# Kernel optimization log

Measured on AMD Instinct MI355X. Metric: run time of the kernel, lower is better.

Reference implementation:

```python
import jax, jax.numpy as jnp
import numpy as np

B, L, D, I = 64, 196, 2048, 512

def setup_inputs() -> dict:
    key = jax.random.key(0)
    ks = jax.random.split(key, 8)
    s_f = 1.0 / np.sqrt(D)
    s_h = 1.0 / np.sqrt(I)
    s_a = 1.0 / np.sqrt(I)
    return {
        "feature_vectors": jax.random.normal(ks[0], (B, L, D), dtype=jnp.float32),
        "hidden_state": jax.random.normal(ks[1], (B, I), dtype=jnp.float32),
        "W_f": jax.random.uniform(ks[2], (D, I), jnp.float32, -s_f, s_f),
        "b_f": jax.random.uniform(ks[3], (I,), jnp.float32, -s_f, s_f),
        "W_h": jax.random.uniform(ks[4], (I, I), jnp.float32, -s_h, s_h),
        "b_h": jax.random.uniform(ks[5], (I,), jnp.float32, -s_h, s_h),
        "W_a": jax.random.uniform(ks[6], (I, D), jnp.float32, -s_a, s_a),
        "b_a": jax.random.uniform(ks[7], (D,), jnp.float32, -s_a, s_a),
    }

def reference(feature_vectors, hidden_state, W_f, b_f, W_h, b_h, W_a, b_a):
    # fv: [B,L,D], hidden: [B,I]
    fv_shaped = jnp.einsum('bld,di->bli', feature_vectors, W_f) + b_f      # [B,L,I]
    hs_shaped = hidden_state @ W_h + b_h                                   # [B,I]
    e = jnp.einsum('bli,id->bld', fv_shaped + hs_shaped[:, None, :], W_a) + b_a  # [B,L,D]
    alpha = jax.nn.softmax(e, axis=1)                                      # softmax over L locations
    z = jnp.sum(alpha * feature_vectors, axis=1)                           # [B,D] (vectorized loop)
    return (z, alpha)
```

## Files before the change

kernel.cpp:

```cpp
#include <hip/hip_runtime.h>

#define B_ 64
#define L_ 196
#define D_ 2048
#define I_ 512
#define M_ (B_*L_)

typedef __attribute__((ext_vector_type(8))) short bf16x8;
typedef __attribute__((ext_vector_type(4))) float f32x4;
typedef unsigned short u16;

__device__ __forceinline__ u16 f2bf(float x){
  unsigned u = __float_as_uint(x);
  u += 0x7fffu + ((u >> 16) & 1u);
  return (u16)(u >> 16);
}

__device__ __forceinline__ void gld16(const void* g, void* l){
  __builtin_amdgcn_global_load_lds(
      (const __attribute__((address_space(1))) void*)g,
      (__attribute__((address_space(3))) void*)l, 16, 0, 0);
}

__global__ void cvt_bf16_kernel(const float* __restrict__ in, u16* __restrict__ out, int n4){
  int i = blockIdx.x*blockDim.x + threadIdx.x;
  int stride = gridDim.x*blockDim.x;
  for (; i < n4; i += stride){
    float4 v = ((const float4*)in)[i];
    ushort4 o;
    o.x = f2bf(v.x); o.y = f2bf(v.y); o.z = f2bf(v.z); o.w = f2bf(v.w);
    ((ushort4*)out)[i] = o;
  }
}

__global__ void transpose_cvt_kernel(const float* __restrict__ in, u16* __restrict__ out, int R, int C){
  __shared__ float tile[32][33];
  int c0 = blockIdx.x*32, r0 = blockIdx.y*32;
  int tx = threadIdx.x, ty = threadIdx.y;
  for (int i=0;i<32;i+=8)
    tile[ty+i][tx] = in[(size_t)(r0+ty+i)*C + c0 + tx];
  __syncthreads();
  for (int i=0;i<32;i+=8)
    out[(size_t)(c0+ty+i)*R + r0 + tx] = f2bf(tile[tx][ty+i]);
}

__global__ void hs_kernel(const float* __restrict__ hidden, const float* __restrict__ Wh,
                          const float* __restrict__ bh, float* __restrict__ hs){
  int n = blockIdx.x*blockDim.x + threadIdx.x;
  int b = blockIdx.y;
  const float* hrow = hidden + b*I_;
  float a0=0.f,a1=0.f,a2=0.f,a3=0.f;
  for (int k=0;k<I_;k+=4){
    a0 = fmaf(hrow[k+0], Wh[(size_t)(k+0)*I_ + n], a0);
    a1 = fmaf(hrow[k+1], Wh[(size_t)(k+1)*I_ + n], a1);
    a2 = fmaf(hrow[k+2], Wh[(size_t)(k+2)*I_ + n], a2);
    a3 = fmaf(hrow[k+3], Wh[(size_t)(k+3)*I_ + n], a3);
  }
  hs[b*I_ + n] = bh[n] + ((a0+a1)+(a2+a3));
}

template<int BN, int K, int MODE, int NLD>
__launch_bounds__(256)
__global__ void gemm_kernel(const u16* __restrict__ A, const u16* __restrict__ Bt,
                            const float* __restrict__ bias, const float* __restrict__ hs,
                            u16* __restrict__ outb, float* __restrict__ outf)
{
  constexpr int BM = 128, BK = 64;
  constexpr int NF = BN/32;
  constexpr int AW = 4;
  constexpr int BW = BN/32;

  __shared__ __align__(16) u16 Als[BM*BK];
  __shared__ __align__(16) u16 Bls[BN*BK];

  const int tid = threadIdx.x, lane = tid & 63, wave = tid >> 6;
  const int m0 = blockIdx.y * BM, n0 = blockIdx.x * BN;
  const int q = lane >> 4, mr = lane & 15;
  const int wrow = (wave & 1) * 64;
  const int wcol = (wave >> 1) * (BN/2);

  const int lrow = lane >> 3;
  const int kc   = (lane & 7) ^ lrow;

  const u16* Ag[AW]; u16* Al[AW];
  #pragma unroll
  for (int u=0; u<AW; ++u){
    int j = wave*AW + u;
    Ag[u] = A + (size_t)(m0 + j*8 + lrow)*K + kc*8;
    Al[u] = Als + j*512;
  }
  const u16* Bg[BW]; u16* Bl[BW];
  #pragma unroll
  for (int u=0; u<BW; ++u){
    int j = wave*BW + u;
    Bg[u] = Bt + (size_t)(n0 + j*8 + lrow)*K + kc*8;
    Bl[u] = Bls + j*512;
  }

  int aoff[4][2], boff[NF][2];
  #pragma unroll
  for (int i=0;i<4;i++)
    #pragma unroll
    for (int s=0;s<2;s++){
      int R = wrow + i*16 + mr;
      aoff[i][s] = R*64 + (((s*4+q) ^ (mr&7))*8);
    }
  #pragma unroll
  for (int j=0;j<NF;j++)
    #pragma unroll
    for (int s=0;s<2;s++){
      int C = wcol + j*16 + mr;
      boff[j][s] = C*64 + (((s*4+q) ^ (mr&7))*8);
    }

  f32x4 acc[4][NF];
  #pragma unroll
  for (int i=0;i<4;i++)
    #pragma unroll
    for (int j=0;j<NF;j++) acc[i][j] = (f32x4){0.f,0.f,0.f,0.f};

  for (int k0=0; k0<K; k0+=BK){
    __syncthreads();
    #pragma unroll
    for (int u=0;u<AW;++u) gld16(Ag[u] + k0, Al[u]);
    #pragma unroll
    for (int u=0;u<BW;++u) gld16(Bg[u] + k0, Bl[u]);
    __syncthreads();
    #pragma unroll
    for (int s=0;s<2;s++){
      bf16x8 af[4], bg[NF];
      #pragma unroll
      for (int i=0;i<4;i++) af[i] = *(const bf16x8*)(Als + aoff[i][s]);
      #pragma unroll
      for (int j=0;j<NF;j++) bg[j] = *(const bf16x8*)(Bls + boff[j][s]);
      #pragma unroll
      for (int i=0;i<4;i++)
        #pragma unroll
        for (int j=0;j<NF;j++)
          acc[i][j] = __builtin_amdgcn_mfma_f32_16x16x32_bf16(af[i], bg[j], acc[i][j], 0,0,0);
    }
  }

  #pragma unroll
  for (int i=0;i<4;i++){
    #pragma unroll
    for (int j=0;j<NF;j++){
      int gcol = n0 + wcol + j*16 + mr;
      float bcol = bias[gcol];
      #pragma unroll
      for (int r=0;r<4;r++){
        int grow = m0 + wrow + i*16 + q*4 + r;
        float v = acc[i][j][r] + bcol;
        if (MODE == 0){
          int batch = grow / L_;
          outb[(size_t)grow*NLD + gcol] = f2bf(v + hs[batch*I_ + gcol]);
        } else {
          outf[(size_t)grow*NLD + gcol] = v;
        }
      }
    }
  }
}

__launch_bounds__(256)
__global__ void softmax_z_kernel(const float* __restrict__ fv, float* __restrict__ out){
  __shared__ float red[4][64];
  const int dl = threadIdx.x & 63, g = threadIdx.x >> 6;
  const int d = blockIdx.x*64 + dl, b = blockIdx.y;
  float* e = out + (size_t)B_*D_ + (size_t)b*L_*D_ + d;
  const float* f = fv + (size_t)b*L_*D_ + d;

  float ev[49];
  float m = -3.4e38f;
  #pragma unroll
  for (int j=0;j<49;j++){
    ev[j] = e[(size_t)(g*49+j)*D_];
    m = fmaxf(m, ev[j]);
  }
  red[g][dl] = m;
  __syncthreads();
  m = fmaxf(fmaxf(red[0][dl],red[1][dl]), fmaxf(red[2][dl],red[3][dl]));
  __syncthreads();

  float s = 0.f;
  #pragma unroll
  for (int j=0;j<49;j++){ ev[j] = __expf(ev[j]-m); s += ev[j]; }
  red[g][dl] = s;
  __syncthreads();
  s = (red[0][dl]+red[1][dl]) + (red[2][dl]+red[3][dl]);
  __syncthreads();

  float inv = 1.f/s, z = 0.f;
  #pragma unroll
  for (int j=0;j<49;j++){
    float a = ev[j]*inv;
    e[(size_t)(g*49+j)*D_] = a;
    z = fmaf(a, f[(size_t)(g*49+j)*D_], z);
  }
  red[g][dl] = z;
  __syncthreads();
  if (g==0)
    out[(size_t)b*D_ + dl + blockIdx.x*64] = (red[0][dl]+red[1][dl]) + (red[2][dl]+red[3][dl]);
}

extern "C" void kernel_launch(void* const* d_in, const int* in_sizes, int n_in,
                              void* d_out, int out_size, void* d_ws, size_t ws_size,
                              hipStream_t stream){
  (void)in_sizes; (void)n_in; (void)out_size; (void)ws_size;
  const float* fv     = (const float*)d_in[0];
  const float* hidden = (const float*)d_in[1];
  const float* W_f    = (const float*)d_in[2];
  const float* b_f    = (const float*)d_in[3];
  const float* W_h    = (const float*)d_in[4];
  const float* b_h    = (const float*)d_in[5];
  const float* W_a    = (const float*)d_in[6];
  const float* b_a    = (const float*)d_in[7];
  float* out = (float*)d_out;

  char* ws = (char*)d_ws;
  u16*   fv_bf = (u16*)ws;
  u16*   t_bf  = (u16*)(ws + 51380224);
  u16*   WfT   = (u16*)(ws + 64225280);
  u16*   WaT   = (u16*)(ws + 66322432);
  float* hsbuf = (float*)(ws + 68419584);

  cvt_bf16_kernel<<<4096, 256, 0, stream>>>(fv, fv_bf, (B_*L_*D_)/4);
  transpose_cvt_kernel<<<dim3(I_/32, D_/32), dim3(32,8), 0, stream>>>(W_f, WfT, D_, I_);
  transpose_cvt_kernel<<<dim3(D_/32, I_/32), dim3(32,8), 0, stream>>>(W_a, WaT, I_, D_);
  hs_kernel<<<dim3(I_/256, B_), 256, 0, stream>>>(hidden, W_h, b_h, hsbuf);

  gemm_kernel<64, D_, 0, I_><<<dim3(I_/64, M_/128), 256, 0, stream>>>(fv_bf, WfT, b_f, hsbuf, t_bf, nullptr);
  gemm_kernel<128, I_, 1, D_><<<dim3(D_/128, M_/128), 256, 0, stream>>>(t_bf, WaT, b_a, nullptr, nullptr, out + B_*D_);

  softmax_z_kernel<<<dim3(D_/64, B_), 256, 0, stream>>>(fv, out);
}
```

Before: 372.3 us.

## Fuse second GEMM with softmax and weighted sum, double-buffer GEMM loads

```diff
diff --git a/kernel.cpp b/kernel.cpp
--- a/kernel.cpp
+++ b/kernel.cpp
@@ -20,6 +20,18 @@
   __builtin_amdgcn_global_load_lds(
       (const __attribute__((address_space(1))) void*)g,
       (__attribute__((address_space(3))) void*)l, 16, 0, 0);
+}
+
+template<int N> __device__ __forceinline__ void wait_vm(){
+  __builtin_amdgcn_s_waitcnt((N&15) | ((N&48)<<10) | (7<<4) | (15<<8));
+}
+__device__ __forceinline__ void wait_lgkm0(){
+  __builtin_amdgcn_s_waitcnt(15 | (48<<10) | (7<<4));
+}
+__device__ __forceinline__ void bar(){
+  asm volatile("" ::: "memory");
+  __builtin_amdgcn_s_barrier();
+  asm volatile("" ::: "memory");
 }
 
 __global__ void cvt_bf16_kernel(const float* __restrict__ in, u16* __restrict__ out, int n4){
@@ -59,148 +71,238 @@
   hs[b*I_ + n] = bh[n] + ((a0+a1)+(a2+a3));
 }
 
-template<int BN, int K, int MODE, int NLD>
 __launch_bounds__(256)
-__global__ void gemm_kernel(const u16* __restrict__ A, const u16* __restrict__ Bt,
-                            const float* __restrict__ bias, const float* __restrict__ hs,
-                            u16* __restrict__ outb, float* __restrict__ outf)
+__global__ void gemm1_kernel(const u16* __restrict__ A, const u16* __restrict__ Bt,
+                             const float* __restrict__ bias, const float* __restrict__ hs,
+                             u16* __restrict__ outb)
 {
-  constexpr int BM = 128, BK = 64;
-  constexpr int NF = BN/32;
-  constexpr int AW = 4;
-  constexpr int BW = BN/32;
-
-  __shared__ __align__(16) u16 Als[BM*BK];
-  __shared__ __align__(16) u16 Bls[BN*BK];
-
-  const int tid = threadIdx.x, lane = tid & 63, wave = tid >> 6;
-  const int m0 = blockIdx.y * BM, n0 = blockIdx.x * BN;
-  const int q = lane >> 4, mr = lane & 15;
-  const int wrow = (wave & 1) * 64;
-  const int wcol = (wave >> 1) * (BN/2);
-
-  const int lrow = lane >> 3;
-  const int kc   = (lane & 7) ^ lrow;
-
-  const u16* Ag[AW]; u16* Al[AW];
-  #pragma unroll
-  for (int u=0; u<AW; ++u){
-    int j = wave*AW + u;
-    Ag[u] = A + (size_t)(m0 + j*8 + lrow)*K + kc*8;
-    Al[u] = Als + j*512;
-  }
-  const u16* Bg[BW]; u16* Bl[BW];
-  #pragma unroll
-  for (int u=0; u<BW; ++u){
-    int j = wave*BW + u;
-    Bg[u] = Bt + (size_t)(n0 + j*8 + lrow)*K + kc*8;
-    Bl[u] = Bls + j*512;
-  }
-
-  int aoff[4][2], boff[NF][2];
-  #pragma unroll
-  for (int i=0;i<4;i++)
+  constexpr int K = D_, BK = 64, NIT = K/BK;
+  __shared__ __align__(16) u16 Als[2][64*64];
+  __shared__ __align__(16) u16 Bls[2][128*64];
+
+  const int tid = threadIdx.x, lane = tid&63, wave = tid>>6;
+  const int m0 = blockIdx.y*64, n0 = blockIdx.x*128;
+  const int q = lane>>4, mr = lane&15;
+  const int wrow = (wave&1)*32, wcol = (wave>>1)*64;
+  const int lrow = lane>>3, kc = (lane&7)^lrow;
+
+  const u16* Ag[2]; int Alo[2];
+  #pragma unroll
+  for (int u=0;u<2;++u){ int j = wave*2+u; Ag[u] = A + (size_t)(m0 + j*8 + lrow)*K + kc*8; Alo[u] = j*512; }
+  const u16* Bg[4]; int Blo[4];
+  #pragma unroll
+  for (int u=0;u<4;++u){ int j = wave*4+u; Bg[u] = Bt + (size_t)(n0 + j*8 + lrow)*K + kc*8; Blo[u] = j*512; }
+
+  int aoff[2][2], boff[4][2];
+  #pragma unroll
+  for (int i=0;i<2;i++)
+    #pragma unroll
+    for (int s=0;s<2;s++){ int R = wrow + i*16 + mr; aoff[i][s] = R*64 + (((s*4+q) ^ (mr&7))*8); }
+  #pragma unroll
+  for (int j=0;j<4;j++)
+    #pragma unroll
+    for (int s=0;s<2;s++){ int C = wcol + j*16 + mr; boff[j][s] = C*64 + (((s*4+q) ^ (mr&7))*8); }
+
+  f32x4 acc[2][4];
+  #pragma unroll
+  for (int i=0;i<2;i++)
+    #pragma unroll
+    for (int j=0;j<4;j++) acc[i][j] = (f32x4){0.f,0.f,0.f,0.f};
+
+  #pragma unroll
+  for (int u=0;u<2;++u) gld16(Ag[u],    &Als[0][Alo[u]]);
+  #pragma unroll
+  for (int u=0;u<4;++u) gld16(Bg[u],    &Bls[0][Blo[u]]);
+  #pragma unroll
+  for (int u=0;u<2;++u) gld16(Ag[u]+BK, &Als[1][Alo[u]]);
+  #pragma unroll
+  for (int u=0;u<4;++u) gld16(Bg[u]+BK, &Bls[1][Blo[u]]);
+
+  for (int i=0;i<NIT;++i){
+    if (i+1<NIT) wait_vm<6>(); else wait_vm<0>();
+    bar();
+    const u16* Ab = Als[i&1];
+    const u16* Bb = Bls[i&1];
+    bf16x8 af[2][2], bg[4][2];
     #pragma unroll
     for (int s=0;s<2;s++){
-      int R = wrow + i*16 + mr;
-      aoff[i][s] = R*64 + (((s*4+q) ^ (mr&7))*8);
-    }
-  #pragma unroll
-  for (int j=0;j<NF;j++)
-    #pragma unroll
-    for (int s=0;s<2;s++){
-      int C = wcol + j*16 + mr;
-      boff[j][s] = C*64 + (((s*4+q) ^ (mr&7))*8);
-    }
-
-  f32x4 acc[4][NF];
-  #pragma unroll
-  for (int i=0;i<4;i++)
-    #pragma unroll
-    for (int j=0;j<NF;j++) acc[i][j] = (f32x4){0.f,0.f,0.f,0.f};
-
-  for (int k0=0; k0<K; k0+=BK){
-    __syncthreads();
-    #pragma unroll
-    for (int u=0;u<AW;++u) gld16(Ag[u] + k0, Al[u]);
-    #pragma unroll
-    for (int u=0;u<BW;++u) gld16(Bg[u] + k0, Bl[u]);
-    __syncthreads();
-    #pragma unroll
-    for (int s=0;s<2;s++){
-      bf16x8 af[4], bg[NF];
-      #pragma unroll
-      for (int i=0;i<4;i++) af[i] = *(const bf16x8*)(Als + aoff[i][s]);
-      #pragma unroll
-      for (int j=0;j<NF;j++) bg[j] = *(const bf16x8*)(Bls + boff[j][s]);
-      #pragma unroll
-      for (int i=0;i<4;i++)
+      #pragma unroll
+      for (int i2=0;i2<2;i2++) af[i2][s] = *(const bf16x8*)(Ab + aoff[i2][s]);
+      #pragma unroll
+      for (int j=0;j<4;j++)    bg[j][s]  = *(const bf16x8*)(Bb + boff[j][s]);
+    }
+    wait_lgkm0();
+    bar();
+    if (i+2<NIT){
+      int k0 = (i+2)*BK;
+      #pragma unroll
+      for (int u=0;u<2;++u) gld16(Ag[u]+k0, &Als[i&1][Alo[u]]);
+      #pragma unroll
+      for (int u=0;u<4;++u) gld16(Bg[u]+k0, &Bls[i&1][Blo[u]]);
+    }
+    #pragma unroll
+    for (int s=0;s<2;s++)
+      #pragma unroll
+      for (int i2=0;i2<2;i2++)
         #pragma unroll
-        for (int j=0;j<NF;j++)
-          acc[i][j] = __builtin_amdgcn_mfma_f32_16x16x32_bf16(af[i], bg[j], acc[i][j], 0,0,0);
-    }
-  }
-
-  #pragma unroll
-  for (int i=0;i<4;i++){
-    #pragma unroll
-    for (int j=0;j<NF;j++){
+        for (int j=0;j<4;j++)
+          acc[i2][j] = __builtin_amdgcn_mfma_f32_16x16x32_bf16(af[i2][s], bg[j][s], acc[i2][j], 0,0,0);
+  }
+
+  #pragma unroll
+  for (int i2=0;i2<2;i2++){
+    #pragma unroll
+    for (int j=0;j<4;j++){
       int gcol = n0 + wcol + j*16 + mr;
       float bcol = bias[gcol];
       #pragma unroll
       for (int r=0;r<4;r++){
-        int grow = m0 + wrow + i*16 + q*4 + r;
-        float v = acc[i][j][r] + bcol;
-        if (MODE == 0){
-          int batch = grow / L_;
-          outb[(size_t)grow*NLD + gcol] = f2bf(v + hs[batch*I_ + gcol]);
-        } else {
-          outf[(size_t)grow*NLD + gcol] = v;
+        int grow = m0 + wrow + i2*16 + q*4 + r;
+        int batch = grow / L_;
+        outb[(size_t)grow*I_ + gcol] = f2bf(acc[i2][j][r] + bcol + hs[batch*I_ + gcol]);
+      }
+    }
+  }
+}
+
+__launch_bounds__(256)
+__global__ void gemm2_fused_kernel(const u16* __restrict__ T, const u16* __restrict__ Wa,
+                                   const float* __restrict__ b_a, const float* __restrict__ fv,
+                                   float* __restrict__ out)
+{
+  constexpr int K = I_, BK = 32, NIT = K/BK;
+  __shared__ __align__(16) u16 Als[2][256*32];
+  __shared__ __align__(16) u16 Bls[2][128*32];
+
+  const int tid = threadIdx.x, lane = tid&63, wave = tid>>6;
+  const int b = blockIdx.y, n0 = blockIdx.x*128;
+  const int q = lane>>4, mr = lane&15;
+  const int wcol = wave*32;
+  const int l16 = lane>>2, kc4 = (lane&3)^(l16&3);
+
+  const u16* Ag[4]; int Alo[4];
+  #pragma unroll
+  for (int u=0;u<4;++u){
+    int j = wave*4+u;
+    int grow = b*L_ + j*16 + l16; if (grow > M_-1) grow = M_-1;
+    Ag[u] = T + (size_t)grow*K + kc4*8; Alo[u] = j*512;
+  }
+  const u16* Bg[2]; int Blo[2];
+  #pragma unroll
+  for (int u=0;u<2;++u){
+    int j = wave*2+u;
+    Bg[u] = Wa + (size_t)(n0 + j*16 + l16)*K + kc4*8; Blo[u] = j*512;
+  }
+
+  const int abase = mr*32 + ((q ^ (mr&3))*8);
+  int boff[2];
+  #pragma unroll
+  for (int j=0;j<2;j++){ int C = wcol + j*16 + mr; boff[j] = C*32 + ((q ^ (mr&3))*8); }
+
+  f32x4 acc[13][2];
+  #pragma unroll
+  for (int i=0;i<13;i++){ acc[i][0] = (f32x4){0,0,0,0}; acc[i][1] = (f32x4){0,0,0,0}; }
+
+  #pragma unroll
+  for (int u=0;u<4;++u) gld16(Ag[u],    &Als[0][Alo[u]]);
+  #pragma unroll
+  for (int u=0;u<2;++u) gld16(Bg[u],    &Bls[0][Blo[u]]);
+  #pragma unroll
+  for (int u=0;u<4;++u) gld16(Ag[u]+BK, &Als[1][Alo[u]]);
+  #pragma unroll
+  for (int u=0;u<2;++u) gld16(Bg[u]+BK, &Bls[1][Blo[u]]);
+
+  for (int it=0; it<NIT; ++it){
+    if (it+1<NIT) wait_vm<6>(); else wait_vm<0>();
+    bar();
+    const u16* Ab = Als[it&1];
+    const u16* Bb = Bls[it&1];
+    bf16x8 bg0 = *(const bf16x8*)(Bb + boff[0]);
+    bf16x8 bg1 = *(const bf16x8*)(Bb + boff[1]);
+    bf16x8 af[13];
+    #pragma unroll
+    for (int i=0;i<13;++i) af[i] = *(const bf16x8*)(Ab + abase + i*512);
+    wait_lgkm0();
+    bar();
+    if (it+2<NIT){
+      int k0 = (it+2)*BK;
+      #pragma unroll
+      for (int u=0;u<4;++u) gld16(Ag[u]+k0, &Als[it&1][Alo[u]]);
+      #pragma unroll
+      for (int u=0;u<2;++u) gld16(Bg[u]+k0, &Bls[it&1][Blo[u]]);
+    }
+    #pragma unroll
+    for (int i=0;i<13;++i){
+      acc[i][0] = __builtin_amdgcn_mfma_f32_16x16x32_bf16(af[i], bg0, acc[i][0], 0,0,0);
+      acc[i][1] = __builtin_amdgcn_mfma_f32_16x16x32_bf16(af[i], bg1, acc[i][1], 0,0,0);
+    }
+  }
+
+  const bool v12 = (q == 0);
+  int col[2] = { n0 + wcol + mr, n0 + wcol + 16 + mr };
+  float bc[2] = { b_a[col[0]], b_a[col[1]] };
+  #pragma unroll
+  for (int i=0;i<13;++i)
+    #pragma unroll
+    for (int j=0;j<2;++j)
+      #pragma unroll
+      for (int r=0;r<4;++r) acc[i][j][r] += bc[j];
+
+  float mx[2], sm[2];
+  #pragma unroll
+  for (int j=0;j<2;++j){
+    float m = -3.4e38f;
+    #pragma unroll
+    for (int i=0;i<12;++i)
+      #pragma unroll
+      for (int r=0;r<4;++r) m = fmaxf(m, acc[i][j][r]);
+    if (v12)
+      #pragma unroll
+      for (int r=0;r<4;++r) m = fmaxf(m, acc[12][j][r]);
+    m = fmaxf(m, __shfl_xor(m, 16));
+    m = fmaxf(m, __shfl_xor(m, 32));
+    mx[j] = m;
+    float s = 0.f;
+    #pragma unroll
+    for (int i=0;i<12;++i)
+      #pragma unroll
+      for (int r=0;r<4;++r){ float e = __expf(acc[i][j][r]-m); acc[i][j][r] = e; s += e; }
+    if (v12)
+      #pragma unroll
+      for (int r=0;r<4;++r){ float e = __expf(acc[12][j][r]-m); acc[12][j][r] = e; s += e; }
+    s += __shfl_xor(s, 16);
+    s += __shfl_xor(s, 32);
+    sm[j] = s;
+  }
+  float inv[2] = { 1.f/sm[0], 1.f/sm[1] };
+
+  float* alpha = out + (size_t)B_*D_ + (size_t)b*L_*D_;
+  const float* fvb = fv + (size_t)b*L_*D_;
+  float z[2] = {0.f, 0.f};
+  #pragma unroll
+  for (int i=0;i<13;++i){
+    if (i < 12 || v12){
+      #pragma unroll
+      for (int r=0;r<4;++r){
+        int row = i*16 + q*4 + r;
+        #pragma unroll
+        for (int j=0;j<2;++j){
+          float a = acc[i][j][r] * inv[j];
+          alpha[(size_t)row*D_ + col[j]] = a;
+          z[j] = fmaf(a, fvb[(size_t)row*D_ + col[j]], z[j]);
         }
       }
     }
   }
-}
-
-__launch_bounds__(256)
-__global__ void softmax_z_kernel(const float* __restrict__ fv, float* __restrict__ out){
-  __shared__ float red[4][64];
-  const int dl = threadIdx.x & 63, g = threadIdx.x >> 6;
-  const int d = blockIdx.x*64 + dl, b = blockIdx.y;
-  float* e = out + (size_t)B_*D_ + (size_t)b*L_*D_ + d;
-  const float* f = fv + (size_t)b*L_*D_ + d;
-
-  float ev[49];
-  float m = -3.4e38f;
-  #pragma unroll
-  for (int j=0;j<49;j++){
-    ev[j] = e[(size_t)(g*49+j)*D_];
-    m = fmaxf(m, ev[j]);
-  }
-  red[g][dl] = m;
-  __syncthreads();
-  m = fmaxf(fmaxf(red[0][dl],red[1][dl]), fmaxf(red[2][dl],red[3][dl]));
-  __syncthreads();
-
-  float s = 0.f;
-  #pragma unroll
-  for (int j=0;j<49;j++){ ev[j] = __expf(ev[j]-m); s += ev[j]; }
-  red[g][dl] = s;
-  __syncthreads();
-  s = (red[0][dl]+red[1][dl]) + (red[2][dl]+red[3][dl]);
-  __syncthreads();
-
-  float inv = 1.f/s, z = 0.f;
-  #pragma unroll
-  for (int j=0;j<49;j++){
-    float a = ev[j]*inv;
-    e[(size_t)(g*49+j)*D_] = a;
-    z = fmaf(a, f[(size_t)(g*49+j)*D_], z);
-  }
-  red[g][dl] = z;
-  __syncthreads();
-  if (g==0)
-    out[(size_t)b*D_ + dl + blockIdx.x*64] = (red[0][dl]+red[1][dl]) + (red[2][dl]+red[3][dl]);
+  #pragma unroll
+  for (int j=0;j<2;++j){
+    z[j] += __shfl_xor(z[j], 16);
+    z[j] += __shfl_xor(z[j], 32);
+  }
+  if (q == 0){
+    out[(size_t)b*D_ + col[0]] = z[0];
+    out[(size_t)b*D_ + col[1]] = z[1];
+  }
 }
 
 extern "C" void kernel_launch(void* const* d_in, const int* in_sizes, int n_in,
@@ -229,8 +331,6 @@
   transpose_cvt_kernel<<<dim3(D_/32, I_/32), dim3(32,8), 0, stream>>>(W_a, WaT, I_, D_);
   hs_kernel<<<dim3(I_/256, B_), 256, 0, stream>>>(hidden, W_h, b_h, hsbuf);
 
-  gemm_kernel<64, D_, 0, I_><<<dim3(I_/64, M_/128), 256, 0, stream>>>(fv_bf, WfT, b_f, hsbuf, t_bf, nullptr);
-  gemm_kernel<128, I_, 1, D_><<<dim3(D_/128, M_/128), 256, 0, stream>>>(t_bf, WaT, b_a, nullptr, nullptr, out + B_*D_);
-
-  softmax_z_kernel<<<dim3(D_/64, B_), 256, 0, stream>>>(fv, out);
-}
+  gemm1_kernel<<<dim3(I_/128, M_/64), 256, 0, stream>>>(fv_bf, WfT, b_f, hsbuf, t_bf);
+  gemm2_fused_kernel<<<dim3(D_/128, B_), 256, 0, stream>>>(t_bf, WaT, b_a, fv, out);
+}
```

Measured after the change: 358.7 us. -3.6%, faster.
